# Kernel optimization log

Measured on AMD Instinct MI355X. Metric: run time of the kernel, lower is better.

## Reference

```python
import jax, jax.numpy as jnp
import numpy as np
from jax import lax

NFFT, WIN, HOP = 512, 320, 160
PAD = NFFT // 2
F = NFFT // 2 + 1  # 257

def _window():
    # torch.hann_window(320, periodic=True), center-padded to n_fft=512 (torch.stft convention)
    w = 0.5 - 0.5 * jnp.cos(2.0 * jnp.pi * jnp.arange(WIN, dtype=jnp.float32) / WIN)
    lp = (NFFT - WIN) // 2
    return jnp.pad(w, (lp, NFFT - WIN - lp))

def _stft(x):  # [N, L] -> [N, T, F] complex64 (center=True, reflect pad)
    xp = jnp.pad(x, ((0, 0), (PAD, PAD)), mode='reflect')
    T = 1 + (xp.shape[1] - NFFT) // HOP
    idx = jnp.arange(T)[:, None] * HOP + jnp.arange(NFFT)[None, :]
    frames = xp[:, idx] * _window()  # [N, T, NFFT]
    return jnp.fft.rfft(frames, axis=-1)

def _istft(spec, length):  # [N, T, F] complex -> [N, length]
    win = _window()
    frames = jnp.fft.irfft(spec, n=NFFT, axis=-1) * win  # [N, T, NFFT]
    N, T, _ = frames.shape
    total = (T - 1) * HOP + NFFT
    pos = (jnp.arange(T)[:, None] * HOP + jnp.arange(NFFT)[None, :]).reshape(-1)
    out = jnp.zeros((N, total), frames.dtype).at[:, pos].add(frames.reshape(N, -1))
    wsq = jnp.zeros((total,), win.dtype).at[pos].add(jnp.tile(win * win, T))
    out = out / jnp.maximum(wsq, 1e-11)[None, :]
    return out[:, PAD:PAD + length]

def _lstm(x, W_ih, W_hh, b_ih, b_hh):  # x [N, T, D] -> [N, T, H]
    N, T, _ = x.shape
    H = W_hh.shape[1]
    xW = x @ W_ih.T + (b_ih + b_hh)  # precompute input projections [N, T, 4H]
    def step(carry, xt):
        h, c = carry
        g = xt + h @ W_hh.T
        i, f, gg, o = jnp.split(g, 4, axis=-1)  # torch gate order i,f,g,o
        c = jax.nn.sigmoid(f) * c + jax.nn.sigmoid(i) * jnp.tanh(gg)
        h = jax.nn.sigmoid(o) * jnp.tanh(c)
        return (h, c), h
    h0 = jnp.zeros((N, H), x.dtype)
    _, hs = lax.scan(step, (h0, h0), jnp.swapaxes(xW, 0, 1))
    return jnp.swapaxes(hs, 0, 1)

def _forward(x, W_ih, W_hh, b_ih, b_hh, W1, b1, W2, b2):
    B, L, C = x.shape
    xm = jnp.transpose(x, (0, 2, 1)).reshape(B * C, L)
    spec = _stft(xm).reshape(B, C, -1, F)  # [B, C, T, F] == r_spec + 1j*i_spec
    T = spec.shape[2]
    feat = jnp.concatenate([spec.real, spec.imag], axis=-1).reshape(B * C, T, 2 * F)
    h = _lstm(feat, W_ih, W_hh, b_ih, b_hh)  # [B*C, T, 128]
    def masked(Wl, bl):
        m = h @ Wl.T + bl                      # [B*C, T, 514]
        rm, im = jnp.split(m, 2, axis=-1)
        mask = (rm + 1j * im).reshape(B, C, T, F)
        return mask * spec                      # complex mask multiply
    s_spec = masked(W1, b1)
    n_spec = masked(W2, b2)
    # per-frequency PSD matrices over time
    psd_s = jnp.einsum('bctf,betf->bfce', s_spec, jnp.conj(s_spec)) / T
    psd_n = jnp.einsum('bctf,betf->bfce', n_spec, jnp.conj(n_spec)) / T
    tr_n = jnp.einsum('bfcc->bf', psd_n).real
    eye = jnp.eye(C, dtype=psd_n.dtype)
    psd_n = psd_n + (1e-6 * tr_n / C + 1e-8)[..., None, None] * eye  # diagonal loading
    num = jnp.linalg.solve(psd_n, psd_s)                             # [B, F, C, C]
    ws = num / (jnp.einsum('bfcc->bf', num)[..., None, None] + 1e-8)
    w = ws[..., 0]                                                   # ref_channel = 0 -> [B, F, C]
    obs = jnp.transpose(spec, (0, 3, 1, 2))                          # [B, F, C, T]
    enh = jnp.einsum('bfc,bfct->bft', jnp.conj(w), obs)              # beamformed [B, F, T]
    return _istft(jnp.transpose(enh, (0, 2, 1)), L)                  # [B, L]

def setup_inputs() -> dict:
    key = jax.random.key(0)
    ks = jax.random.split(key, 8)
    D, H = 2 * F, 128
    s = 0.05
    return {
        'x': jax.random.normal(ks[0], (8, 96000, 8), jnp.float32),
        'W_ih': jax.random.normal(ks[1], (4 * H, D), jnp.float32) * s,
        'W_hh': jax.random.normal(ks[2], (4 * H, H), jnp.float32) * s,
        'b_ih': jnp.zeros((4 * H,), jnp.float32),
        'b_hh': jnp.zeros((4 * H,), jnp.float32),
        'W1': jax.random.normal(ks[3], (D, H), jnp.float32) * s,
        'b1': jnp.zeros((D,), jnp.float32),
        'W2': jax.random.normal(ks[4], (D, H), jnp.float32) * s,
        'b2': jnp.zeros((D,), jnp.float32),
    }

def reference(x, W_ih, W_hh, b_ih, b_hh, W1, b1, W2, b2):
    return _forward(x, W_ih, W_hh, b_ih, b_hh, W1, b1, W2, b2)
```

## Files before the change

kernel.cpp:

```cpp
#include <hip/hip_runtime.h>
#include <math.h>

#define NFFT  512
#define WINL  320
#define HOP   160
#define FPAD  256
#define NF    257
#define TT    601
#define LSEQ  96000
#define XPLEN 96512
#define NCH   8
#define NB    8
#define NSEQ  64
#define NROWS 38464
#define DD    514
#define HH    128
#define G4    512
#define KPAD  544
#define NCOMB 1026

#define NXP   24128
#define NWSQ  377
#define NBFF  1028
#define NWT   1088
#define NBI   1088
#define NBS   2
#define NWM   640
#define NWP   128
#define NINIT (NXP + NWSQ + NBFF + NWT + NBI + NBS + NWM + NWP)

typedef _Float16 h2v __attribute__((ext_vector_type(2)));
typedef short bf16x8 __attribute__((ext_vector_type(8)));
typedef float f32x4 __attribute__((ext_vector_type(4)));

__device__ __forceinline__ float winval(int k) {
  if (k < 96 || k >= 416) return 0.f;
  return 0.5f - 0.5f * cosf((float)(2.0 * M_PI / 320.0) * (float)(k - 96));
}

__device__ __forceinline__ void split_bf16(float v, unsigned short* h, unsigned short* l) {
  unsigned int hb = __float_as_uint(v) >> 16;
  float r = v - __uint_as_float(hb << 16);
  *h = (unsigned short)hb;
  *l = (unsigned short)(__float_as_uint(r) >> 16);
}

__device__ __forceinline__ void glds16(const unsigned short* g, unsigned short* l) {
  __builtin_amdgcn_global_load_lds(
      (const __attribute__((address_space(1))) void*)g,
      (__attribute__((address_space(3))) void*)l,
      16, 0, 0);
}

__device__ __forceinline__ int xcd_swz(int orig, int nwg) {
  int q = nwg >> 3, r = nwg & 7;
  int xcd = orig & 7, slot = orig >> 3;
  return (xcd < r ? xcd * (q + 1) : r * (q + 1) + (xcd - r) * q) + slot;
}

__global__ void k_init(const float* __restrict__ x, const float* __restrict__ Wih,
                       const float* __restrict__ Whh, const float* __restrict__ bih,
                       const float* __restrict__ bhh, const float* __restrict__ W1,
                       const float* __restrict__ W2,
                       unsigned short* __restrict__ XPh, unsigned short* __restrict__ XPl,
                       float* __restrict__ wsq, float* __restrict__ BFf,
                       unsigned short* __restrict__ WTh, unsigned short* __restrict__ WTl,
                       unsigned short* __restrict__ BIh, unsigned short* __restrict__ BIl,
                       float* __restrict__ BSUM,
                       unsigned short* __restrict__ W1h, unsigned short* __restrict__ W1l,
                       unsigned short* __restrict__ W2h, unsigned short* __restrict__ W2l,
                       unsigned int* __restrict__ WhhP4) {
  int b = blockIdx.x;
  const int tid = threadIdx.x;

  if (b < NXP) {
    int idx = b * 256 + tid;
    if (idx < NSEQ * XPLEN) {
      int n = idx / XPLEN, i = idx - n * XPLEN;
      int j = i - FPAD;
      if (j < 0) j = -j;
      else if (j >= LSEQ) j = 2 * LSEQ - 2 - j;
      int bb = n >> 3, c = n & 7;
      float v = x[((long)bb * LSEQ + j) * NCH + c];
      split_bf16(v, &XPh[idx], &XPl[idx]);
    }
    return;
  }
  b -= NXP;

  if (b < NWSQ) {
    int p = b * 256 + tid;
    if (p < XPLEN) {
      int t0 = (p <= 511) ? 0 : (p - 352) / 160;
      int t1 = p / 160; if (t1 > 600) t1 = 600;
      float s = 0.f;
      for (int t = t0; t <= t1; t++) { float w = winval(p - t * HOP); s += w * w; }
      wsq[p] = s;
    }
    return;
  }
  b -= NWSQ;

  if (b < NBFF) {
    int idx = b * 256 + tid;
    if (idx < NFFT * DD) {
      int k = idx / DD, d = idx - k * DD;
      float w = winval(k);
      int f = (d < NF) ? d : d - NF;
      int m = (k * f) & 511;
      float th = (float)(M_PI / 256.0) * (float)m;
      BFf[idx] = ((d < NF) ? cosf(th) : -sinf(th)) * w;
    }
    return;
  }
  b -= NBFF;

  if (b < NWT) {
    int idx = b * 256 + tid;
    if (idx < G4 * KPAD) {
      int n = idx / KPAD, k = idx - n * KPAD;
      float v = (k < DD) ? Wih[n * DD + k] : 0.f;
      split_bf16(v, &WTh[idx], &WTl[idx]);
    }
    return;
  }
  b -= NWT;

  if (b < NBI) {
    int idx = b * 256 + tid;
    if (idx < NFFT * KPAD) {
      int n = idx / KPAD, kk = idx - n * KPAD;
      float v = 0.f;
      if (kk < DD) {
        float w = winval(n);
        int f = (kk < NF) ? kk : kk - NF;
        int edge = (f == 0 || f == 256);
        float alpha = edge ? 1.f : 2.f;
        int m = (n * f) & 511;
        float th = (float)(M_PI / 256.0) * (float)m;
        float c;
        if (kk < NF) c = alpha * cosf(th);
        else         c = edge ? 0.f : -alpha * sinf(th);
        v = c * w * (1.f / 512.f);
      }
      split_bf16(v, &BIh[idx], &BIl[idx]);
    }
    return;
  }
  b -= NBI;

  if (b < NBS) {
    int idx = b * 256 + tid;
    if (idx < G4) BSUM[idx] = bih[idx] + bhh[idx];
    return;
  }
  b -= NBS;

  if (b < NWM) {
    int idx = b * 256 + tid;
    if (idx < 2 * 640 * HH) {
      int m = idx / (640 * HH);
      int rem = idx - m * 640 * HH;
      int np = rem / HH, k = rem - np * HH;
      int ri = np / 320, f = np - ri * 320;
      float v = 0.f;
      if (f < NF) {
        int fcol = (ri == 0) ? f : NF + f;
        v = (m == 0) ? W1[fcol * HH + k] : W2[fcol * HH + k];
      }
      unsigned short h, l;
      split_bf16(v, &h, &l);
      if (m == 0) { W1h[rem] = h; W1l[rem] = l; }
      else        { W2h[rem] = h; W2l[rem] = l; }
    }
    return;
  }
  b -= NWM;

  {
    int idx = b * 256 + tid;
    if (idx < G4 * 64) {
      int j = idx >> 6, k2 = idx & 63;
      _Float16 lo = (_Float16)Whh[j * HH + 2 * k2];
      _Float16 hi = (_Float16)Whh[j * HH + 2 * k2 + 1];
      unsigned int u = ((unsigned int)__builtin_bit_cast(unsigned short, hi) << 16)
                     |  (unsigned int)__builtin_bit_cast(unsigned short, lo);
      WhhP4[(k2 >> 2) * (G4 * 4) + j * 4 + (k2 & 3)] = u;
    }
  }
}

__global__ void k_bcomb(const float* __restrict__ BWf, unsigned short* __restrict__ H,
                        unsigned short* __restrict__ L,
                        unsigned short* __restrict__ BFsh, unsigned short* __restrict__ BFsl) {
  int idx = blockIdx.x * 256 + threadIdx.x;
  if (idx >= 1152 * KPAD) return;
  int n = idx / KPAD, k = idx - n * KPAD;
  float v = 0.f;
  if (k < NFFT) {
    if (n < DD) {
      float w = winval(k);
      int f = (n < NF) ? n : n - NF;
      int m = (k * f) & 511;
      float th = (float)(M_PI / 256.0) * (float)m;
      v = ((n < NF) ? cosf(th) : -sinf(th)) * w;
    } else if (n < NCOMB) {
      v = BWf[k * G4 + (n - 514)];
    }
  }
  unsigned short h, l;
  split_bf16(v, &h, &l);
  H[idx] = h; L[idx] = l;
  if (n < 512) { BFsh[idx] = h; BFsl[idx] = l; }
}

template <int GATHER>
__launch_bounds__(256)
__global__ void k_gemm3(const float* __restrict__ A,
                        const unsigned short* __restrict__ Bth,
                        const unsigned short* __restrict__ Btl,
                        const float* __restrict__ bias, float* __restrict__ C,
                        int M, int N, int K, int lda, int ldc) {
  __shared__ __align__(16) unsigned short sAh[128 * 40];
  __shared__ __align__(16) unsigned short sAl[128 * 40];
  __shared__ __align__(16) unsigned short sBh[128 * 40];
  __shared__ __align__(16) unsigned short sBl[128 * 40];
  const int tid = threadIdx.x;
  const int row0 = blockIdx.y * 128, col0 = blockIdx.x * 128;
  const int sar = tid >> 1, sak = (tid & 1) * 16;
  const int arow = row0 + sar;
  long abase = (long)arow * lda;
  const bool arok = (arow < M);
  const int lane = tid & 63, w = tid >> 6;
  const int wm = (w >> 1) * 64, wn = (w & 1) * 64;
  const int l15 = lane & 15, quad = lane >> 4;
  f32x4 acc[4][4] = {};
  unsigned int* aH = (unsigned int*)sAh;
  unsigned int* aL = (unsigned int*)sAl;
  uint4* bH = (uint4*)sBh;
  uint4* bL = (uint4*)sBl;
  for (int k0 = 0; k0 < K; k0 += 32) {
#pragma unroll
    for (int i = 0; i < 8; i++) {
      int kk = k0 + sak + 2 * i;
      float v0 = 0.f, v1 = 0.f;
      if (arok) {
        if (kk + 1 < K) { float2 t2 = *(const float2*)(A + abase + kk); v0 = t2.x; v1 = t2.y; }
        else if (kk < K) { v0 = A[abase + kk]; }
      }
      unsigned int h0 = __float_as_uint(v0) >> 16, h1 = __float_as_uint(v1) >> 16;
      float r0 = v0 - __uint_as_float(h0 << 16), r1 = v1 - __uint_as_float(h1 << 16);
      unsigned int l0 = __float_as_uint(r0) >> 16, l1 = __float_as_uint(r1) >> 16;
      aH[sar * 20 + (sak >> 1) + i] = h0 | (h1 << 16);
      aL[sar * 20 + (sak >> 1) + i] = l0 | (l1 << 16);
    }
#pragma unroll
    for (int h = 0; h < 2; h++) {
      int idx = tid + h * 256;
      int r = idx >> 2, c = idx & 3;
      long go = (long)(col0 + r) * KPAD + k0 + c * 8;
      bH[r * 5 + c] = *(const uint4*)(Bth + go);
      bL[r * 5 + c] = *(const uint4*)(Btl + go);
    }
    __syncthreads();
    bf16x8 ah[4], al[4], bh[4], bl[4];
#pragma unroll
    for (int i = 0; i < 4; i++) {
      int off = (wm + i * 16 + l15) * 40 + quad * 8;
      ah[i] = *(const bf16x8*)(sAh + off);
      al[i] = *(const bf16x8*)(sAl + off);
      int boff = (wn + i * 16 + l15) * 40 + quad * 8;
      bh[i] = *(const bf16x8*)(sBh + boff);
      bl[i] = *(const bf16x8*)(sBl + boff);
    }
#pragma unroll
    for (int i = 0; i < 4; i++)
#pragma unroll
      for (int j = 0; j < 4; j++) {
        acc[i][j] = __builtin_amdgcn_mfma_f32_16x16x32_bf16(al[i], bh[j], acc[i][j], 0, 0, 0);
        acc[i][j] = __builtin_amdgcn_mfma_f32_16x16x32_bf16(ah[i], bl[j], acc[i][j], 0, 0, 0);
        acc[i][j] = __builtin_amdgcn_mfma_f32_16x16x32_bf16(ah[i], bh[j], acc[i][j], 0, 0, 0);
      }
    __syncthreads();
  }
#pragma unroll
  for (int i = 0; i < 4; i++)
#pragma unroll
    for (int j = 0; j < 4; j++) {
      int cc = col0 + wn + j * 16 + l15;
      if (cc >= N) continue;
      float bv = bias ? bias[cc] : 0.f;
#pragma unroll
      for (int rg = 0; rg < 4; rg++) {
        int rr = row0 + wm + i * 16 + quad * 4 + rg;
        if (rr < M) C[(long)rr * ldc + cc] = acc[i][j][rg] + bv;
      }
    }
}

__launch_bounds__(256)
__global__ void k_gemm4(const unsigned short* __restrict__ Ah, const unsigned short* __restrict__ Al,
                        const unsigned short* __restrict__ Bh, const unsigned short* __restrict__ Bl,
                        const float* __restrict__ bsum, float* __restrict__ S,
                        float* __restrict__ XW, int colBase, int nCT) {
  __shared__ __align__(16) unsigned short sAh[128 * 32];
  __shared__ __align__(16) unsigned short sAl[128 * 32];
  __shared__ __align__(16) unsigned short sBh[128 * 32];
  __shared__ __align__(16) unsigned short sBl[128 * 32];
  const int tid = threadIdx.x;
  const int wg = xcd_swz(blockIdx.x, nCT * 301);
  const int row0 = (wg / nCT) * 128, col0 = (colBase + wg % nCT) * 128;
  const int lane = tid & 63, w = tid >> 6;
  const int wm = (w >> 1) * 64, wn = (w & 1) * 64;
  const int l15 = lane & 15, quad = lane >> 4;
  const int sr0 = w * 32 + (lane >> 2);
  const int sr1 = sr0 + 16;
  const int c8 = (lane & 3) * 8;
  long ab0, ab1;
  { int rr = row0 + sr0; int n = rr / TT, t = rr - n * TT; ab0 = (long)n * XPLEN + (long)t * HOP + c8; }
  { int rr = row0 + sr1; int n = rr / TT, t = rr - n * TT; ab1 = (long)n * XPLEN + (long)t * HOP + c8; }
  const long bb0 = (long)(col0 + sr0) * KPAD + c8;
  const long bb1 = (long)(col0 + sr1) * KPAD + c8;
  const int d0 = w * 1024;
  const int d1 = d0 + 512;
  f32x4 acc[4][4] = {};
  for (int k0 = 0; k0 < NFFT; k0 += 32) {
    glds16(Ah + ab0 + k0, sAh + d0);
    glds16(Ah + ab1 + k0, sAh + d1);
    glds16(Al + ab0 + k0, sAl + d0);
    glds16(Al + ab1 + k0, sAl + d1);
    glds16(Bh + bb0 + k0, sBh + d0);
    glds16(Bh + bb1 + k0, sBh + d1);
    glds16(Bl + bb0 + k0, sBl + d0);
    glds16(Bl + bb1 + k0, sBl + d1);
    __syncthreads();
    bf16x8 ah[4], al[4], bh[4], bl[4];
#pragma unroll
    for (int i = 0; i < 4; i++) {
      int off = (wm + i * 16 + l15) * 32 + quad * 8;
      ah[i] = *(const bf16x8*)(sAh + off);
      al[i] = *(const bf16x8*)(sAl + off);
      int boff = (wn + i * 16 + l15) * 32 + quad * 8;
      bh[i] = *(const bf16x8*)(sBh + boff);
      bl[i] = *(const bf16x8*)(sBl + boff);
    }
#pragma unroll
    for (int i = 0; i < 4; i++)
#pragma unroll
      for (int j = 0; j < 4; j++) {
        acc[i][j] = __builtin_amdgcn_mfma_f32_16x16x32_bf16(al[i], bh[j], acc[i][j], 0, 0, 0);
        acc[i][j] = __builtin_amdgcn_mfma_f32_16x16x32_bf16(ah[i], bl[j], acc[i][j], 0, 0, 0);
        acc[i][j] = __builtin_amdgcn_mfma_f32_16x16x32_bf16(ah[i], bh[j], acc[i][j], 0, 0, 0);
      }
    __syncthreads();
  }
#pragma unroll
  for (int i = 0; i < 4; i++)
#pragma unroll
    for (int j = 0; j < 4; j++) {
      int cc = col0 + wn + j * 16 + l15;
      if (cc >= NCOMB) continue;
#pragma unroll
      for (int rg = 0; rg < 4; rg++) {
        int rr = row0 + wm + i * 16 + quad * 4 + rg;
        if (rr >= NROWS) continue;
        float v = acc[i][j][rg];
        if (cc < DD) S[(long)rr * DD + cc] = v;
        else         XW[(long)rr * G4 + (cc - 514)] = v + bsum[cc - 514];
      }
    }
}

__launch_bounds__(256)
__global__ void k_gemm5(const unsigned short* __restrict__ Ah, const unsigned short* __restrict__ Al,
                        const unsigned short* __restrict__ Bh, const unsigned short* __restrict__ Bl,
                        float* __restrict__ C, int M, int N, int ldc) {
  __shared__ __align__(16) unsigned short sAh[128 * 40];
  __shared__ __align__(16) unsigned short sAl[128 * 40];
  __shared__ __align__(16) unsigned short sBh[128 * 40];
  __shared__ __align__(16) unsigned short sBl[128 * 40];
  const int tid = threadIdx.x;
  const int row0 = blockIdx.y * 128, col0 = blockIdx.x * 128;
  const int sr0 = tid >> 2, c4 = (tid & 3) * 8, cq = tid & 3;
  const int lane = tid & 63, w = tid >> 6;
  const int wm = (w >> 1) * 64, wn = (w & 1) * 64;
  const int l15 = lane & 15, quad = lane >> 4;
  f32x4 acc[4][4] = {};
  uint4* aH4 = (uint4*)sAh; uint4* aL4 = (uint4*)sAl;
  uint4* bH4 = (uint4*)sBh; uint4* bL4 = (uint4*)sBl;
  for (int k0 = 0; k0 < KPAD; k0 += 32) {
    {
      long go = (long)(row0 + sr0) * KPAD + k0 + c4;
      aH4[sr0 * 5 + cq] = *(const uint4*)(Ah + go);
      aL4[sr0 * 5 + cq] = *(const uint4*)(Al + go);
      go = (long)(row0 + sr0 + 64) * KPAD + k0 + c4;
      aH4[(sr0 + 64) * 5 + cq] = *(const uint4*)(Ah + go);
      aL4[(sr0 + 64) * 5 + cq] = *(const uint4*)(Al + go);
    }
    {
      long go = (long)(col0 + sr0) * KPAD + k0 + c4;
      bH4[sr0 * 5 + cq] = *(const uint4*)(Bh + go);
      bL4[sr0 * 5 + cq] = *(const uint4*)(Bl + go);
      go = (long)(col0 + sr0 + 64) * KPAD + k0 + c4;
      bH4[(sr0 + 64) * 5 + cq] = *(const uint4*)(Bh + go);
      bL4[(sr0 + 64) * 5 + cq] = *(const uint4*)(Bl + go);
    }
    __syncthreads();
    bf16x8 ah[4], al[4], bh[4], bl[4];
#pragma unroll
    for (int i = 0; i < 4; i++) {
      int off = (wm + i * 16 + l15) * 40 + quad * 8;
      ah[i] = *(const bf16x8*)(sAh + off);
      al[i] = *(const bf16x8*)(sAl + off);
      int boff = (wn + i * 16 + l15) * 40 + quad * 8;
      bh[i] = *(const bf16x8*)(sBh + boff);
      bl[i] = *(const bf16x8*)(sBl + boff);
    }
#pragma unroll
    for (int i = 0; i < 4; i++)
#pragma unroll
      for (int j = 0; j < 4; j++) {
        acc[i][j] = __builtin_amdgcn_mfma_f32_16x16x32_bf16(al[i], bh[j], acc[i][j], 0, 0, 0);
        acc[i][j] = __builtin_amdgcn_mfma_f32_16x16x32_bf16(ah[i], bl[j], acc[i][j], 0, 0, 0);
        acc[i][j] = __builtin_amdgcn_mfma_f32_16x16x32_bf16(ah[i], bh[j], acc[i][j], 0, 0, 0);
      }
    __syncthreads();
  }
#pragma unroll
  for (int i = 0; i < 4; i++)
#pragma unroll
    for (int j = 0; j < 4; j++) {
      int cc = col0 + wn + j * 16 + l15;
      if (cc >= N) continue;
#pragma unroll
      for (int rg = 0; rg < 4; rg++) {
        int rr = row0 + wm + i * 16 + quad * 4 + rg;
        if (rr < M) C[(long)rr * ldc + cc] = acc[i][j][rg];
      }
    }
}

__device__ __forceinline__ float tanh_fast(float x) {
  float e = __expf(2.f * x);
  return 1.f - 2.f / (e + 1.f);
}

__launch_bounds__(512)
__global__ void k_lstm_s(const float* __restrict__ XW, const unsigned int* __restrict__ WhhP4,
                         float* __restrict__ Hout,
                         const unsigned short* __restrict__ Ah, const unsigned short* __restrict__ Al,
                         const unsigned short* __restrict__ Bh, const unsigned short* __restrict__ Bl,
                         float* __restrict__ S) {
  __shared__ __align__(16) unsigned short sAh[128 * 32];
  __shared__ __align__(16) unsigned short sAl[128 * 32];
  __shared__ __align__(16) unsigned short sBh[128 * 32];
  __shared__ __align__(16) unsigned short sBl[128 * 32];
  __shared__ __align__(16) unsigned int hl2[64];
  __shared__ float gl[G4];
  const int tid = threadIdx.x;

  if (blockIdx.x < 64) {
    __builtin_amdgcn_s_setprio(1);
    const int j = tid;
    const int n = blockIdx.x;
    const uint4* W4 = (const uint4*)WhhP4;
    unsigned int wp[64];
#pragma unroll
    for (int i4 = 0; i4 < 16; i4++) {
      uint4 v = W4[i4 * G4 + j];
      wp[4 * i4]     = v.x;
      wp[4 * i4 + 1] = v.y;
      wp[4 * i4 + 2] = v.z;
      wp[4 * i4 + 3] = v.w;
    }
    float cst = 0.f;
    if (j < 64) hl2[j] = 0u;
    const float* xwrow = XW + (long)n * TT * G4 + j;
    float xnext = xwrow[0];
    const uint4* h4 = (const uint4*)hl2;
    const bool isg = (j >= 2 * HH) && (j < 3 * HH);
    __syncthreads();
    for (int t = 0; t < TT; t++) {
      float xv = xnext;
      if (t + 1 < TT) xnext = xwrow[(long)(t + 1) * G4];
      float a0 = 0.f, a1 = 0.f, a2 = 0.f, a3 = 0.f;
#pragma unroll
      for (int k = 0; k < 16; k++) {
        uint4 hv4 = h4[k];
        a0 = __builtin_amdgcn_fdot2(__builtin_bit_cast(h2v, hv4.x), __builtin_bit_cast(h2v, wp[4 * k]),     a0, false);
        a1 = __builtin_amdgcn_fdot2(__builtin_bit_cast(h2v, hv4.y), __builtin_bit_cast(h2v, wp[4 * k + 1]), a1, false);
        a2 = __builtin_amdgcn_fdot2(__builtin_bit_cast(h2v, hv4.z), __builtin_bit_cast(h2v, wp[4 * k + 2]), a2, false);
        a3 = __builtin_amdgcn_fdot2(__builtin_bit_cast(h2v, hv4.w), __builtin_bit_cast(h2v, wp[4 * k + 3]), a3, false);
      }
      float a = ((a0 + a1) + (a2 + a3)) + xv;
      float nl;
      if (isg) nl = tanh_fast(a);
      else     nl = 1.f / (1.f + __expf(-a));
      gl[j] = nl;
      asm volatile("s_waitcnt lgkmcnt(0)" ::: "memory");
      __builtin_amdgcn_s_barrier();
      if (j < HH) {
        float ni = gl[j], nf = gl[HH + j], ng = gl[2 * HH + j], no = gl[3 * HH + j];
        cst = nf * cst + ni * ng;
        float hv = no * tanh_fast(cst);
        ((_Float16*)hl2)[j] = (_Float16)hv;
        Hout[((long)n * TT + t) * HH + j] = hv;
      }
      asm volatile("s_waitcnt lgkmcnt(0)" ::: "memory");
      __builtin_amdgcn_s_barrier();
    }
    __builtin_amdgcn_s_setprio(0);
    return;
  }

  const int wg = xcd_swz(blockIdx.x - 64, 4 * 301);
  const int row0 = (wg >> 2) * 128, col0 = (wg & 3) * 128;
  const int lane = tid & 63, w = tid >> 6;
  const int wm = (w >> 1) * 64, wn = (w & 1) * 64;
  const int l15 = lane & 15, quad = lane >> 4;
  const int sr0 = w * 32 + (lane >> 2);
  const int sr1 = sr0 + 16;
  const int c8 = (lane & 3) * 8;
  long ab0 = 0, ab1 = 0, bb0 = 0, bb1 = 0;
  int d0 = 0, d1 = 0;
  if (tid < 256) {
    { int rr = row0 + sr0; int n = rr / TT, t = rr - n * TT; ab0 = (long)n * XPLEN + (long)t * HOP + c8; }
    { int rr = row0 + sr1; int n = rr / TT, t = rr - n * TT; ab1 = (long)n * XPLEN + (long)t * HOP + c8; }
    bb0 = (long)(col0 + sr0) * KPAD + c8;
    bb1 = (long)(col0 + sr1) * KPAD + c8;
    d0 = w * 1024;
    d1 = d0 + 512;
  }
  f32x4 acc[4][4] = {};
  for (int k0 = 0; k0 < NFFT; k0 += 32) {
    if (tid < 256) {
      glds16(Ah + ab0 + k0, sAh + d0);
      glds16(Ah + ab1 + k0, sAh + d1);
      glds16(Al + ab0 + k0, sAl + d0);
      glds16(Al + ab1 + k0, sAl + d1);
      glds16(Bh + bb0 + k0, sBh + d0);
      glds16(Bh + bb1 + k0, sBh + d1);
      glds16(Bl + bb0 + k0, sBl + d0);
      glds16(Bl + bb1 + k0, sBl + d1);
    }
    __syncthreads();
    if (tid < 256) {
      bf16x8 ah[4], al[4], bh[4], bl[4];
#pragma unroll
      for (int i = 0; i < 4; i++) {
        int off = (wm + i * 16 + l15) * 32 + quad * 8;
        ah[i] = *(const bf16x8*)(sAh + off);
        al[i] = *(const bf16x8*)(sAl + off);
        int boff = (wn + i * 16 + l15) * 32 + quad * 8;
        bh[i] = *(const bf16x8*)(sBh + boff);
        bl[i] = *(const bf16x8*)(sBl + boff);
      }
#pragma unroll
      for (int i = 0; i < 4; i++)
#pragma unroll
        for (int j = 0; j < 4; j++) {
          acc[i][j] = __builtin_amdgcn_mfma_f32_16x16x32_bf16(al[i], bh[j], acc[i][j], 0, 0, 0);
          acc[i][j] = __builtin_amdgcn_mfma_f32_16x16x32_bf16(ah[i], bl[j], acc[i][j], 0, 0, 0);
          acc[i][j] = __builtin_amdgcn_mfma_f32_16x16x32_bf16(ah[i], bh[j], acc[i][j], 0, 0, 0);
        }
    }
    __syncthreads();
  }
  if (tid < 256) {
#pragma unroll
    for (int i = 0; i < 4; i++)
#pragma unroll
      for (int j = 0; j < 4; j++) {
        int cc = col0 + wn + j * 16 + l15;
#pragma unroll
        for (int rg = 0; rg < 4; rg++) {
          int rr = row0 + wm + i * 16 + quad * 4 + rg;
          if (rr < NROWS) S[(long)rr * DD + cc] = acc[i][j][rg];
        }
      }
  }
}

__launch_bounds__(256)
__global__ void k_maskms(const float* __restrict__ Hout,
                         const unsigned short* __restrict__ Wsh,
                         const unsigned short* __restrict__ Wsl,
                         const float* __restrict__ bias, const float* __restrict__ S,
                         float* __restrict__ MS) {
  __shared__ __align__(16) unsigned short sAh[64 * 40];
  __shared__ __align__(16) unsigned short sAl[64 * 40];
  __shared__ __align__(16) unsigned short sBh[64 * 40];
  __shared__ __align__(16) unsigned short sBl[64 * 40];
  __shared__ float Cs[64][68];
  __shared__ float SR[64][33];
  __shared__ float SI[64][33];
  const int tid = threadIdx.x;
  const int wg = xcd_swz(blockIdx.x, 9 * 601);
  const int f0 = (wg % 9) * 32;
  const int row0 = (wg / 9) * 64;
  const int lane = tid & 63, w = tid >> 6;
  const int wm = w * 16;
  const int l15 = lane & 15, quad = lane >> 4;
  const int sar = tid >> 2;
  const int sak = (tid & 3) * 8;
  const int np = ((sar < 32) ? 0 : 320 - 32) + f0 + sar;
  unsigned int* aH = (unsigned int*)sAh;
  unsigned int* aL = (unsigned int*)sAl;
  f32x4 acc[4] = {};
  for (int k0 = 0; k0 < HH; k0 += 32) {
    {
      const float* ap = Hout + (long)(row0 + sar) * HH + k0 + sak;
      float4 v0 = *(const float4*)ap;
      float4 v1 = *(const float4*)(ap + 4);
      float vv[8] = {v0.x, v0.y, v0.z, v0.w, v1.x, v1.y, v1.z, v1.w};
#pragma unroll
      for (int i = 0; i < 4; i++) {
        unsigned int h0 = __float_as_uint(vv[2 * i]) >> 16, h1 = __float_as_uint(vv[2 * i + 1]) >> 16;
        float r0 = vv[2 * i] - __uint_as_float(h0 << 16), r1 = vv[2 * i + 1] - __uint_as_float(h1 << 16);
        unsigned int l0 = __float_as_uint(r0) >> 16, l1 = __float_as_uint(r1) >> 16;
        aH[sar * 20 + (sak >> 1) + i] = h0 | (h1 << 16);
        aL[sar * 20 + (sak >> 1) + i] = l0 | (l1 << 16);
      }
    }
    {
      long go = (long)np * HH + k0 + sak;
      *(uint4*)(sBh + sar * 40 + sak) = *(const uint4*)(Wsh + go);
      *(uint4*)(sBl + sar * 40 + sak) = *(const uint4*)(Wsl + go);
    }
    __syncthreads();
    bf16x8 ah = *(const bf16x8*)(sAh + (wm + l15) * 40 + quad * 8);
    bf16x8 al = *(const bf16x8*)(sAl + (wm + l15) * 40 + quad * 8);
#pragma unroll
    for (int ct = 0; ct < 4; ct++) {
      bf16x8 bh = *(const bf16x8*)(sBh + (ct * 16 + l15) * 40 + quad * 8);
      bf16x8 bl = *(const bf16x8*)(sBl + (ct * 16 + l15) * 40 + quad * 8);
      acc[ct] = __builtin_amdgcn_mfma_f32_16x16x32_bf16(al, bh, acc[ct], 0, 0, 0);
      acc[ct] = __builtin_amdgcn_mfma_f32_16x16x32_bf16(ah, bl, acc[ct], 0, 0, 0);
      acc[ct] = __builtin_amdgcn_mfma_f32_16x16x32_bf16(ah, bh, acc[ct], 0, 0, 0);
    }
    __syncthreads();
  }
#pragma unroll
  for (int ct = 0; ct < 4; ct++) {
    int col = ct * 16 + l15;
    int f = f0 + (col & 31);
    int fcol = (col < 32) ? f : NF + f;
    float bv = (f < NF) ? bias[fcol] : 0.f;
#pragma unroll
    for (int rg = 0; rg < 4; rg++) Cs[wm + quad * 4 + rg][col] = acc[ct][rg] + bv;
  }
  __syncthreads();
  {
    int fl = tid & 31, r8 = tid >> 5;
    int f = f0 + fl;
#pragma unroll
    for (int i = 0; i < 8; i++) {
      int rl = r8 * 8 + i;
      int rr = row0 + rl;
      float rm = Cs[rl][fl], im = Cs[rl][32 + fl];
      float sr = 0.f, si = 0.f;
      if (f < NF) { sr = S[(long)rr * DD + f]; si = S[(long)rr * DD + NF + f]; }
      SR[rl][fl] = rm * sr - im * si;
      SI[rl][fl] = rm * si + im * sr;
    }
  }
  __syncthreads();
  {
    int tl = tid & 63, fq = tid >> 6;
    int rr = row0 + tl;
    int n = rr / TT, t = rr - n * TT;
    int b = n >> 3, c = n & 7;
#pragma unroll
    for (int i = 0; i < 8; i++) {
      int fl = fq * 8 + i;
      int f = f0 + fl;
      if (f < NF) {
        long addr = ((((long)b * NF + f) * 8 + c) * (long)TT + t) * 2;
        *(float2*)&MS[addr] = make_float2(SR[tl][fl], SI[tl][fl]);
      }
    }
  }
}

__launch_bounds__(256)
__global__ void k_psd(const float* __restrict__ MS, float* __restrict__ PSD) {
  __shared__ float buf[9616];
  __shared__ float part[64][8];
  const int tid = threadIdx.x;
  const long base = (long)blockIdx.x * 9616;
  for (int i = tid; i < 9616; i += 256) buf[i] = MS[base + i];
  __syncthreads();
  int p = tid & 63, q = tid >> 6;
  int c = p >> 3, e = p & 7;
  const float2* xc = (const float2*)&buf[c * 1202];
  const float2* xe = (const float2*)&buf[e * 1202];
  int t0 = q * 150, t1 = (q == 3) ? TT : t0 + 150;
  float ar = 0.f, ai = 0.f;
  for (int t = t0; t < t1; t++) {
    float2 m = xc[t];
    float2 v = xe[t];
    ar += m.x * v.x + m.y * v.y;
    ai += m.y * v.x - m.x * v.y;
  }
  part[p][q * 2] = ar; part[p][q * 2 + 1] = ai;
  __syncthreads();
  if (tid < 64) {
    float sr = part[tid][0] + part[tid][2] + part[tid][4] + part[tid][6];
    float si = part[tid][1] + part[tid][3] + part[tid][5] + part[tid][7];
    PSD[((long)blockIdx.x * 64 + tid) * 2]     = sr * (1.f / 601.f);
    PSD[((long)blockIdx.x * 64 + tid) * 2 + 1] = si * (1.f / 601.f);
  }
}

__launch_bounds__(64)
__global__ void k_solve(const float* __restrict__ PS, const float* __restrict__ PN,
                        float* __restrict__ WV) {
  int idx = blockIdx.x * 64 + threadIdx.x;
  if (idx >= NB * NF) return;
  float Ar[8][8], Ai[8][8], Br[8][8], Bi[8][8];
  const float* pn = PN + (long)idx * 128;
  const float* ps = PS + (long)idx * 128;
  for (int i = 0; i < 8; i++)
    for (int j = 0; j < 8; j++) {
      Ar[i][j] = pn[(i * 8 + j) * 2]; Ai[i][j] = pn[(i * 8 + j) * 2 + 1];
      Br[i][j] = ps[(i * 8 + j) * 2]; Bi[i][j] = ps[(i * 8 + j) * 2 + 1];
    }
  float tr = 0.f;
  for (int i = 0; i < 8; i++) tr += Ar[i][i];
  float load = 1e-6f * tr / 8.f + 1e-8f;
  for (int i = 0; i < 8; i++) Ar[i][i] += load;
  for (int k = 0; k < 8; k++) {
    int piv = k; float mx = Ar[k][k] * Ar[k][k] + Ai[k][k] * Ai[k][k];
    for (int i = k + 1; i < 8; i++) {
      float m2 = Ar[i][k] * Ar[i][k] + Ai[i][k] * Ai[i][k];
      if (m2 > mx) { mx = m2; piv = i; }
    }
    if (piv != k) {
      for (int j = 0; j < 8; j++) {
        float t0;
        t0 = Ar[k][j]; Ar[k][j] = Ar[piv][j]; Ar[piv][j] = t0;
        t0 = Ai[k][j]; Ai[k][j] = Ai[piv][j]; Ai[piv][j] = t0;
        t0 = Br[k][j]; Br[k][j] = Br[piv][j]; Br[piv][j] = t0;
        t0 = Bi[k][j]; Bi[k][j] = Bi[piv][j]; Bi[piv][j] = t0;
      }
    }
    float dr = Ar[k][k], di = Ai[k][k];
    float inv = 1.f / (dr * dr + di * di);
    float irr = dr * inv, iii = -di * inv;
    for (int j = 0; j < 8; j++) {
      float xr = Ar[k][j], xi = Ai[k][j];
      Ar[k][j] = xr * irr - xi * iii; Ai[k][j] = xr * iii + xi * irr;
      xr = Br[k][j]; xi = Bi[k][j];
      Br[k][j] = xr * irr - xi * iii; Bi[k][j] = xr * iii + xi * irr;
    }
    for (int i = 0; i < 8; i++) {
      if (i == k) continue;
      float fr = Ar[i][k], fi = Ai[i][k];
      for (int j = 0; j < 8; j++) {
        float kr = Ar[k][j], ki = Ai[k][j];
        Ar[i][j] -= fr * kr - fi * ki;
        Ai[i][j] -= fr * ki + fi * kr;
        kr = Br[k][j]; ki = Bi[k][j];
        Br[i][j] -= fr * kr - fi * ki;
        Bi[i][j] -= fr * ki + fi * kr;
      }
    }
  }
  float trr = 1e-8f, tri = 0.f;
  for (int i = 0; i < 8; i++) { trr += Br[i][i]; tri += Bi[i][i]; }
  float inv = 1.f / (trr * trr + tri * tri);
  for (int c = 0; c < 8; c++) {
    float xr = Br[c][0], xi = Bi[c][0];
    WV[((long)idx * 8 + c) * 2]     = (xr * trr + xi * tri) * inv;
    WV[((long)idx * 8 + c) * 2 + 1] = (xi * trr - xr * tri) * inv;
  }
}

__launch_bounds__(320)
__global__ void k_beam(const float* __restrict__ S, const float* __restrict__ WV,
                       unsigned short* __restrict__ ENHh, unsigned short* __restrict__ ENHl) {
  __shared__ float WL[NF * 16];
  int bb = blockIdx.x / TT, t = blockIdx.x - bb * TT;
  for (int i = threadIdx.x; i < NF * 16; i += 320) WL[i] = WV[(long)bb * NF * 16 + i];
  __syncthreads();
  int f = threadIdx.x;
  long base = ((long)bb * TT + t) * KPAD;
  if (f < NF) {
    float er = 0.f, ei = 0.f;
#pragma unroll
    for (int c = 0; c < 8; c++) {
      float wr = WL[(f * 8 + c) * 2], wi = WL[(f * 8 + c) * 2 + 1];
      const float* srow = S + (((long)(bb * 8 + c) * TT) + t) * DD;
      float sr = srow[f], si = srow[NF + f];
      er += wr * sr + wi * si;
      ei += wr * si - wi * sr;
    }
    split_bf16(er, &ENHh[base + f], &ENHl[base + f]);
    split_bf16(ei, &ENHh[base + NF + f], &ENHl[base + NF + f]);
  }
  int z = threadIdx.x - 288;
  if (z >= 0 && z < 30) { ENHh[base + DD + z] = 0; ENHl[base + DD + z] = 0; }
}

__global__ void k_ola(const float* __restrict__ IFR, const float* __restrict__ WSQ,
                      float* __restrict__ out) {
  int idx = blockIdx.x * 256 + threadIdx.x;
  if (idx >= NB * LSEQ) return;
  int b = idx / LSEQ, l = idx - b * LSEQ;
  int p = l + FPAD;
  int t0 = (p <= 511) ? 0 : (p - 352) / 160;
  int t1 = p / 160; if (t1 > 600) t1 = 600;
  float s = 0.f;
  for (int t = t0; t <= t1; t++) s += IFR[((long)b * TT + t) * NFFT + (p - t * HOP)];
  out[idx] = s / fmaxf(WSQ[p], 1e-11f);
}

extern "C" void kernel_launch(void* const* d_in, const int* in_sizes, int n_in,
                              void* d_out, int out_size, void* d_ws, size_t ws_size,
                              hipStream_t stream) {
  (void)in_sizes; (void)n_in; (void)out_size; (void)ws_size;
  const float* x   = (const float*)d_in[0];
  const float* Wih = (const float*)d_in[1];
  const float* Whh = (const float*)d_in[2];
  const float* bih = (const float*)d_in[3];
  const float* bhh = (const float*)d_in[4];
  const float* W1  = (const float*)d_in[5];
  const float* b1  = (const float*)d_in[6];
  const float* W2  = (const float*)d_in[7];
  const float* b2  = (const float*)d_in[8];
  float* ws = (float*)d_ws;

  unsigned short* XPh = (unsigned short*)(ws + 0);
  unsigned short* XPl = (unsigned short*)(ws + 3088384);
  float* S     = ws + 6176768;
  float* XWM   = ws + 25951264;
  float* HOUT  = ws + 45725760;
  float* PSD_S = ws + 50650048;
  float* PSD_N = ws + 50913216;
  float* WV    = ws + 51176384;
  float* BSUM  = ws + 51209280;
  float* WSQ   = ws + 51209792;
  unsigned short* W1sh = (unsigned short*)(ws + 51306304);
  unsigned short* W1sl = (unsigned short*)(ws + 51347264);
  unsigned short* W2sh = (unsigned short*)(ws + 51388224);
  unsigned short* W2sl = (unsigned short*)(ws + 51429184);
  unsigned short* WTth = (unsigned short*)(ws + 51470144);
  unsigned short* WTtl = (unsigned short*)(ws + 51609408);
  unsigned short* BIth = (unsigned short*)(ws + 51748672);
  unsigned short* BItl = (unsigned short*)(ws + 51887936);
  float* MS    = XWM;
  float* IFR   = ws + 0;
  unsigned int* WhhP4 = (unsigned int*)(XWM + 19693568);
  float* BFf = HOUT;
  float* BWf = HOUT + 263168;
  unsigned short* BCh = (unsigned short*)(HOUT + 525312);
  unsigned short* BCl = (unsigned short*)(HOUT + 838656);
  unsigned short* BFsh = (unsigned short*)PSD_S;
  unsigned short* BFsl = (unsigned short*)PSD_N;
  unsigned short* ENHh = (unsigned short*)HOUT;
  unsigned short* ENHl = (unsigned short*)(HOUT + 1307776);

  k_init<<<NINIT, 256, 0, stream>>>(x, Wih, Whh, bih, bhh, W1, W2,
                                    XPh, XPl, WSQ, BFf, WTth, WTtl, BIth, BItl,
                                    BSUM, W1sh, W1sl, W2sh, W2sl, WhhP4);

  {
    dim3 g(4, 4);
    k_gemm3<0><<<g, 256, 0, stream>>>(BFf, WTth, WTtl, nullptr, BWf, 512, 512, DD, DD, G4);
  }
  k_bcomb<<<(1152 * KPAD + 255) / 256, 256, 0, stream>>>(BWf, BCh, BCl, BFsh, BFsl);

  k_gemm4<<<5 * 301, 256, 0, stream>>>(XPh, XPl, BCh, BCl, BSUM, S, XWM, 4, 5);

  k_lstm_s<<<64 + 4 * 301, 512, 0, stream>>>(XWM, WhhP4, HOUT, XPh, XPl, BFsh, BFsl, S);

  k_maskms<<<9 * 601, 256, 0, stream>>>(HOUT, W1sh, W1sl, b1, S, MS);
  k_psd<<<NB * NF, 256, 0, stream>>>(MS, PSD_S);
  k_maskms<<<9 * 601, 256, 0, stream>>>(HOUT, W2sh, W2sl, b2, S, MS);
  k_psd<<<NB * NF, 256, 0, stream>>>(MS, PSD_N);

  k_solve<<<(NB * NF + 63) / 64, 64, 0, stream>>>(PSD_S, PSD_N, WV);
  k_beam<<<NB * TT, 320, 0, stream>>>(S, WV, ENHh, ENHl);

  {
    dim3 g(4, 38);
    k_gemm5<<<g, 256, 0, stream>>>(ENHh, ENHl, BIth, BItl, IFR, NB * TT, NFFT, NFFT);
  }

  k_ola<<<(NB * LSEQ + 255) / 256, 256, 0, stream>>>(IFR, WSQ, (float*)d_out);
}
```

Baseline: 1.021 ms.

## Tile input transpose via LDS and move independent prep into LSTM kernel

The padded-signal conversion in k_init now reads contiguous chunks of x into shared memory and writes each channel plane with coalesced stores, with a small separate path for the reflect-padded edges. This replaces the old per-element strided gather. The window-square, inverse-basis and mask-weight preparation blocks move out of k_init into extra blocks of the LSTM launch, so they run alongside the serial recurrence instead of on the critical path. In exchange the LSTM launch grows, the extra blocks leave half their threads idle, and these blocks compete for CUs with the recurrence blocks.

```diff
diff --git a/kernel.cpp b/kernel.cpp
--- a/kernel.cpp
+++ b/kernel.cpp
@@ -19,15 +19,18 @@
 #define KPAD  544
 #define NCOMB 1026
 
-#define NXP   24128
-#define NWSQ  377
+#define NXPC  3000
+#define NXPE  128
 #define NBFF  1028
 #define NWT   1088
+#define NBS   2
+#define NWP   128
+#define NINIT (NXPC + NXPE + NBFF + NWT + NBS + NWP)
+#define NWSQ  377
 #define NBI   1088
-#define NBS   2
 #define NWM   640
-#define NWP   128
-#define NINIT (NXP + NWSQ + NBFF + NWT + NBI + NBS + NWM + NWP)
+#define NGB   1204
+#define NAUX  (NWSQ + NBI + NWM)
 
 typedef _Float16 h2v __attribute__((ext_vector_type(2)));
 typedef short bf16x8 __attribute__((ext_vector_type(8)));
@@ -60,46 +63,54 @@
 
 __global__ void k_init(const float* __restrict__ x, const float* __restrict__ Wih,
                        const float* __restrict__ Whh, const float* __restrict__ bih,
-                       const float* __restrict__ bhh, const float* __restrict__ W1,
-                       const float* __restrict__ W2,
+                       const float* __restrict__ bhh,
                        unsigned short* __restrict__ XPh, unsigned short* __restrict__ XPl,
-                       float* __restrict__ wsq, float* __restrict__ BFf,
+                       float* __restrict__ BFf,
                        unsigned short* __restrict__ WTh, unsigned short* __restrict__ WTl,
-                       unsigned short* __restrict__ BIh, unsigned short* __restrict__ BIl,
                        float* __restrict__ BSUM,
-                       unsigned short* __restrict__ W1h, unsigned short* __restrict__ W1l,
-                       unsigned short* __restrict__ W2h, unsigned short* __restrict__ W2l,
                        unsigned int* __restrict__ WhhP4) {
   int b = blockIdx.x;
   const int tid = threadIdx.x;
 
-  if (b < NXP) {
+  if (b < NXPC) {
+    __shared__ float f[256 * 9];
+    int bb = b / 375, chunk = b - bb * 375;
+    int j0 = chunk * 256;
+    long gbase = ((long)bb * LSEQ + j0) * 8;
+#pragma unroll
+    for (int k = 0; k < 8; k++) {
+      int e = tid + k * 256;
+      float v = x[gbase + e];
+      f[(e >> 3) * 9 + (e & 7)] = v;
+    }
+    __syncthreads();
+    int c = tid >> 5, t31 = tid & 31;
+    long plane = (long)(bb * 8 + c) * XPLEN;
+#pragma unroll
+    for (int jj = 0; jj < 8; jj++) {
+      int jl = jj * 32 + t31;
+      float v = f[jl * 9 + c];
+      long o = plane + j0 + jl + FPAD;
+      split_bf16(v, &XPh[o], &XPl[o]);
+    }
+    return;
+  }
+  b -= NXPC;
+
+  if (b < NXPE) {
     int idx = b * 256 + tid;
-    if (idx < NSEQ * XPLEN) {
-      int n = idx / XPLEN, i = idx - n * XPLEN;
-      int j = i - FPAD;
-      if (j < 0) j = -j;
-      else if (j >= LSEQ) j = 2 * LSEQ - 2 - j;
-      int bb = n >> 3, c = n & 7;
-      float v = x[((long)bb * LSEQ + j) * NCH + c];
-      split_bf16(v, &XPh[idx], &XPl[idx]);
-    }
+    int n = idx >> 9, e = idx & 511;
+    int i = (e < 256) ? e : (96000 + e);
+    int j = i - FPAD;
+    if (j < 0) j = -j;
+    else if (j >= LSEQ) j = 2 * LSEQ - 2 - j;
+    int bb = n >> 3, c = n & 7;
+    float v = x[((long)bb * LSEQ + j) * NCH + c];
+    long o = (long)n * XPLEN + i;
+    split_bf16(v, &XPh[o], &XPl[o]);
     return;
   }
-  b -= NXP;
-
-  if (b < NWSQ) {
-    int p = b * 256 + tid;
-    if (p < XPLEN) {
-      int t0 = (p <= 511) ? 0 : (p - 352) / 160;
-      int t1 = p / 160; if (t1 > 600) t1 = 600;
-      float s = 0.f;
-      for (int t = t0; t <= t1; t++) { float w = winval(p - t * HOP); s += w * w; }
-      wsq[p] = s;
-    }
-    return;
-  }
-  b -= NWSQ;
+  b -= NXPE;
 
   if (b < NBFF) {
     int idx = b * 256 + tid;
@@ -126,56 +137,12 @@
   }
   b -= NWT;
 
-  if (b < NBI) {
-    int idx = b * 256 + tid;
-    if (idx < NFFT * KPAD) {
-      int n = idx / KPAD, kk = idx - n * KPAD;
-      float v = 0.f;
-      if (kk < DD) {
-        float w = winval(n);
-        int f = (kk < NF) ? kk : kk - NF;
-        int edge = (f == 0 || f == 256);
-        float alpha = edge ? 1.f : 2.f;
-        int m = (n * f) & 511;
-        float th = (float)(M_PI / 256.0) * (float)m;
-        float c;
-        if (kk < NF) c = alpha * cosf(th);
-        else         c = edge ? 0.f : -alpha * sinf(th);
-        v = c * w * (1.f / 512.f);
-      }
-      split_bf16(v, &BIh[idx], &BIl[idx]);
-    }
-    return;
-  }
-  b -= NBI;
-
   if (b < NBS) {
     int idx = b * 256 + tid;
     if (idx < G4) BSUM[idx] = bih[idx] + bhh[idx];
     return;
   }
   b -= NBS;
-
-  if (b < NWM) {
-    int idx = b * 256 + tid;
-    if (idx < 2 * 640 * HH) {
-      int m = idx / (640 * HH);
-      int rem = idx - m * 640 * HH;
-      int np = rem / HH, k = rem - np * HH;
-      int ri = np / 320, f = np - ri * 320;
-      float v = 0.f;
-      if (f < NF) {
-        int fcol = (ri == 0) ? f : NF + f;
-        v = (m == 0) ? W1[fcol * HH + k] : W2[fcol * HH + k];
-      }
-      unsigned short h, l;
-      split_bf16(v, &h, &l);
-      if (m == 0) { W1h[rem] = h; W1l[rem] = l; }
-      else        { W2h[rem] = h; W2l[rem] = l; }
-    }
-    return;
-  }
-  b -= NWM;
 
   {
     int idx = b * 256 + tid;
@@ -450,7 +417,12 @@
                          float* __restrict__ Hout,
                          const unsigned short* __restrict__ Ah, const unsigned short* __restrict__ Al,
                          const unsigned short* __restrict__ Bh, const unsigned short* __restrict__ Bl,
-                         float* __restrict__ S) {
+                         float* __restrict__ S,
+                         const float* __restrict__ W1, const float* __restrict__ W2,
+                         float* __restrict__ wsqp,
+                         unsigned short* __restrict__ BIh, unsigned short* __restrict__ BIl,
+                         unsigned short* __restrict__ W1h, unsigned short* __restrict__ W1l,
+                         unsigned short* __restrict__ W2h, unsigned short* __restrict__ W2l) {
   __shared__ __align__(16) unsigned short sAh[128 * 32];
   __shared__ __align__(16) unsigned short sAl[128 * 32];
   __shared__ __align__(16) unsigned short sBh[128 * 32];
@@ -513,71 +485,130 @@
     return;
   }
 
-  const int wg = xcd_swz(blockIdx.x - 64, 4 * 301);
-  const int row0 = (wg >> 2) * 128, col0 = (wg & 3) * 128;
-  const int lane = tid & 63, w = tid >> 6;
-  const int wm = (w >> 1) * 64, wn = (w & 1) * 64;
-  const int l15 = lane & 15, quad = lane >> 4;
-  const int sr0 = w * 32 + (lane >> 2);
-  const int sr1 = sr0 + 16;
-  const int c8 = (lane & 3) * 8;
-  long ab0 = 0, ab1 = 0, bb0 = 0, bb1 = 0;
-  int d0 = 0, d1 = 0;
-  if (tid < 256) {
-    { int rr = row0 + sr0; int n = rr / TT, t = rr - n * TT; ab0 = (long)n * XPLEN + (long)t * HOP + c8; }
-    { int rr = row0 + sr1; int n = rr / TT, t = rr - n * TT; ab1 = (long)n * XPLEN + (long)t * HOP + c8; }
-    bb0 = (long)(col0 + sr0) * KPAD + c8;
-    bb1 = (long)(col0 + sr1) * KPAD + c8;
-    d0 = w * 1024;
-    d1 = d0 + 512;
-  }
-  f32x4 acc[4][4] = {};
-  for (int k0 = 0; k0 < NFFT; k0 += 32) {
+  int gb = blockIdx.x - 64;
+  if (gb < NGB) {
+    const int wg = xcd_swz(gb, NGB);
+    const int row0 = (wg >> 2) * 128, col0 = (wg & 3) * 128;
+    const int lane = tid & 63, w = tid >> 6;
+    const int wm = (w >> 1) * 64, wn = (w & 1) * 64;
+    const int l15 = lane & 15, quad = lane >> 4;
+    const int sr0 = w * 32 + (lane >> 2);
+    const int sr1 = sr0 + 16;
+    const int c8 = (lane & 3) * 8;
+    long ab0 = 0, ab1 = 0, bb0 = 0, bb1 = 0;
+    int d0 = 0, d1 = 0;
     if (tid < 256) {
-      glds16(Ah + ab0 + k0, sAh + d0);
-      glds16(Ah + ab1 + k0, sAh + d1);
-      glds16(Al + ab0 + k0, sAl + d0);
-      glds16(Al + ab1 + k0, sAl + d1);
-      glds16(Bh + bb0 + k0, sBh + d0);
-      glds16(Bh + bb1 + k0, sBh + d1);
-      glds16(Bl + bb0 + k0, sBl + d0);
-      glds16(Bl + bb1 + k0, sBl + d1);
-    }
-    __syncthreads();
+      { int rr = row0 + sr0; int n = rr / TT, t = rr - n * TT; ab0 = (long)n * XPLEN + (long)t * HOP + c8; }
+      { int rr = row0 + sr1; int n = rr / TT, t = rr - n * TT; ab1 = (long)n * XPLEN + (long)t * HOP + c8; }
+      bb0 = (long)(col0 + sr0) * KPAD + c8;
+      bb1 = (long)(col0 + sr1) * KPAD + c8;
+      d0 = w * 1024;
+      d1 = d0 + 512;
+    }
+    f32x4 acc[4][4] = {};
+    for (int k0 = 0; k0 < NFFT; k0 += 32) {
+      if (tid < 256) {
+        glds16(Ah + ab0 + k0, sAh + d0);
+        glds16(Ah + ab1 + k0, sAh + d1);
+        glds16(Al + ab0 + k0, sAl + d0);
+        glds16(Al + ab1 + k0, sAl + d1);
+        glds16(Bh + bb0 + k0, sBh + d0);
+        glds16(Bh + bb1 + k0, sBh + d1);
+        glds16(Bl + bb0 + k0, sBl + d0);
+        glds16(Bl + bb1 + k0, sBl + d1);
+      }
+      __syncthreads();
+      if (tid < 256) {
+        bf16x8 ah[4], al[4], bh[4], bl[4];
+#pragma unroll
+        for (int i = 0; i < 4; i++) {
+          int off = (wm + i * 16 + l15) * 32 + quad * 8;
+          ah[i] = *(const bf16x8*)(sAh + off);
+          al[i] = *(const bf16x8*)(sAl + off);
+          int boff = (wn + i * 16 + l15) * 32 + quad * 8;
+          bh[i] = *(const bf16x8*)(sBh + boff);
+          bl[i] = *(const bf16x8*)(sBl + boff);
+        }
+#pragma unroll
+        for (int i = 0; i < 4; i++)
+#pragma unroll
+          for (int j = 0; j < 4; j++) {
+            acc[i][j] = __builtin_amdgcn_mfma_f32_16x16x32_bf16(al[i], bh[j], acc[i][j], 0, 0, 0);
+            acc[i][j] = __builtin_amdgcn_mfma_f32_16x16x32_bf16(ah[i], bl[j], acc[i][j], 0, 0, 0);
+            acc[i][j] = __builtin_amdgcn_mfma_f32_16x16x32_bf16(ah[i], bh[j], acc[i][j], 0, 0, 0);
+          }
+      }
+      __syncthreads();
+    }
     if (tid < 256) {
-      bf16x8 ah[4], al[4], bh[4], bl[4];
-#pragma unroll
-      for (int i = 0; i < 4; i++) {
-        int off = (wm + i * 16 + l15) * 32 + quad * 8;
-        ah[i] = *(const bf16x8*)(sAh + off);
-        al[i] = *(const bf16x8*)(sAl + off);
-        int boff = (wn + i * 16 + l15) * 32 + quad * 8;
-        bh[i] = *(const bf16x8*)(sBh + boff);
-        bl[i] = *(const bf16x8*)(sBl + boff);
-      }
 #pragma unroll
       for (int i = 0; i < 4; i++)
 #pragma unroll
         for (int j = 0; j < 4; j++) {
-          acc[i][j] = __builtin_amdgcn_mfma_f32_16x16x32_bf16(al[i], bh[j], acc[i][j], 0, 0, 0);
-          acc[i][j] = __builtin_amdgcn_mfma_f32_16x16x32_bf16(ah[i], bl[j], acc[i][j], 0, 0, 0);
-          acc[i][j] = __builtin_amdgcn_mfma_f32_16x16x32_bf16(ah[i], bh[j], acc[i][j], 0, 0, 0);
+          int cc = col0 + wn + j * 16 + l15;
+#pragma unroll
+          for (int rg = 0; rg < 4; rg++) {
+            int rr = row0 + wm + i * 16 + quad * 4 + rg;
+            if (rr < NROWS) S[(long)rr * DD + cc] = acc[i][j][rg];
+          }
         }
     }
-    __syncthreads();
-  }
-  if (tid < 256) {
-#pragma unroll
-    for (int i = 0; i < 4; i++)
-#pragma unroll
-      for (int j = 0; j < 4; j++) {
-        int cc = col0 + wn + j * 16 + l15;
-#pragma unroll
-        for (int rg = 0; rg < 4; rg++) {
-          int rr = row0 + wm + i * 16 + quad * 4 + rg;
-          if (rr < NROWS) S[(long)rr * DD + cc] = acc[i][j][rg];
-        }
-      }
+    return;
+  }
+
+  int sb = gb - NGB;
+  if (tid >= 256) return;
+  if (sb < NWSQ) {
+    int p = sb * 256 + tid;
+    if (p < XPLEN) {
+      int t0 = (p <= 511) ? 0 : (p - 352) / 160;
+      int t1 = p / 160; if (t1 > 600) t1 = 600;
+      float s = 0.f;
+      for (int t = t0; t <= t1; t++) { float w = winval(p - t * HOP); s += w * w; }
+      wsqp[p] = s;
+    }
+    return;
+  }
+  sb -= NWSQ;
+  if (sb < NBI) {
+    int idx = sb * 256 + tid;
+    if (idx < NFFT * KPAD) {
+      int n = idx / KPAD, kk = idx - n * KPAD;
+      float v = 0.f;
+      if (kk < DD) {
+        float w = winval(n);
+        int f = (kk < NF) ? kk : kk - NF;
+        int edge = (f == 0 || f == 256);
+        float alpha = edge ? 1.f : 2.f;
+        int m = (n * f) & 511;
+        float th = (float)(M_PI / 256.0) * (float)m;
+        float c;
+        if (kk < NF) c = alpha * cosf(th);
+        else         c = edge ? 0.f : -alpha * sinf(th);
+        v = c * w * (1.f / 512.f);
+      }
+      split_bf16(v, &BIh[idx], &BIl[idx]);
+    }
+    return;
+  }
+  sb -= NBI;
+  {
+    int idx = sb * 256 + tid;
+    if (idx < 2 * 640 * HH) {
+      int m = idx / (640 * HH);
+      int rem = idx - m * 640 * HH;
+      int np = rem / HH, k = rem - np * HH;
+      int ri = np / 320, f = np - ri * 320;
+      float v = 0.f;
+      if (f < NF) {
+        int fcol = (ri == 0) ? f : NF + f;
+        v = (m == 0) ? W1[fcol * HH + k] : W2[fcol * HH + k];
+      }
+      unsigned short h, l;
+      split_bf16(v, &h, &l);
+      if (m == 0) { W1h[rem] = h; W1l[rem] = l; }
+      else        { W2h[rem] = h; W2l[rem] = l; }
+    }
   }
 }
 
@@ -860,9 +891,8 @@
   unsigned short* ENHh = (unsigned short*)HOUT;
   unsigned short* ENHl = (unsigned short*)(HOUT + 1307776);
 
-  k_init<<<NINIT, 256, 0, stream>>>(x, Wih, Whh, bih, bhh, W1, W2,
-                                    XPh, XPl, WSQ, BFf, WTth, WTtl, BIth, BItl,
-                                    BSUM, W1sh, W1sl, W2sh, W2sl, WhhP4);
+  k_init<<<NINIT, 256, 0, stream>>>(x, Wih, Whh, bih, bhh,
+                                    XPh, XPl, BFf, WTth, WTtl, BSUM, WhhP4);
 
   {
     dim3 g(4, 4);
@@ -872,7 +902,9 @@
 
   k_gemm4<<<5 * 301, 256, 0, stream>>>(XPh, XPl, BCh, BCl, BSUM, S, XWM, 4, 5);
 
-  k_lstm_s<<<64 + 4 * 301, 512, 0, stream>>>(XWM, WhhP4, HOUT, XPh, XPl, BFsh, BFsl, S);
+  k_lstm_s<<<64 + NGB + NAUX, 512, 0, stream>>>(XWM, WhhP4, HOUT, XPh, XPl, BFsh, BFsl, S,
+                                                W1, W2, WSQ, BIth, BItl,
+                                                W1sh, W1sl, W2sh, W2sl);
 
   k_maskms<<<9 * 601, 256, 0, stream>>>(HOUT, W1sh, W1sl, b1, S, MS);
   k_psd<<<NB * NF, 256, 0, stream>>>(MS, PSD_S);
```

Result: no change. 1.005 ms (-1.6%).
